# Optimization experiments

Measured on AMD Instinct MI355X. Metric: run time of the kernel, lower is better.

Reference implementation:

```python
import jax, jax.numpy as jnp
import numpy as np

# Dims (match init_kwargs)
T, C, RF, L = 32, 1, 64, 4096   # timesteps, inchannels, rf_size, length
K2 = 512                        # out_channels of self.ec
KWTA = 8
THRESH2 = 0.2                   # thresholds[1]
# inhibition_radius = 0 -> only per-feature inhibition in the winner loop


def setup_inputs() -> dict:
    key = jax.random.key(0)
    k1, k2 = jax.random.split(key)
    # spike-wave style input in [0,1)
    rec_field = jax.random.uniform(k1, (T, C, RF, L), dtype=jnp.float32)
    fan_in = C * RF * L
    weight = jax.random.normal(k2, (K2, C, RF, L), dtype=jnp.float32) / np.float32(np.sqrt(fan_in))
    return {"rec_field": rec_field, "weight": weight}


def reference(rec_field, weight):
    # LocalConvolution with kernel == full input -> single output location:
    # out[t, o, 0, 0] = sum_{c,h,w} rec_field[t,c,h,w] * weight[o,c,h,w]
    out = jnp.einsum('tchw,ochw->to', rec_field, weight)[:, :, None, None]  # (T, K2, 1, 1)

    # sf.fire(out, thresh2, True): zero potentials strictly below threshold
    pot = jnp.where(out < THRESH2, jnp.zeros_like(out), out)
    spikes = jnp.sign(pot)  # pot >= 0 after thresholding -> spikes in {0,1}

    # sf.get_k_winners(pot, kwta, inhibition_radius): spikes = pot.sign()
    n_t = spikes.shape[0]
    # index of earliest spike time (SpykeTorch cumulative-spike convention)
    first = jnp.clip((n_t - spikes.sum(axis=0, keepdims=True)).astype(jnp.int32), 0, n_t - 1)
    values = jnp.take_along_axis(pot, first, axis=0)          # (1, K2, 1, 1)
    trunc = spikes * values                                   # propagate earliest potential
    v = trunc.max() * n_t                                     # large offset so spiking neurons dominate
    trunc = trunc + spikes * v
    total = trunc.sum(axis=0)[:, 0, 0]                        # (K2,) -- spatial dims are 1x1

    # iterative k-WTA with per-feature inhibition (inhibition_radius=0; spatial is 1x1)
    sel = jnp.zeros((K2,), dtype=bool)
    t = total
    for _ in range(KWTA):  # small static loop
        idx = jnp.argmax(t)
        valid = t[idx] != 0          # original breaks when max == 0; totals are >= 0
        sel = sel.at[idx].set(sel[idx] | valid)
        t = t.at[idx].set(0.0)       # inhibit winning feature

    coef = sel.astype(pot.dtype)[None, :, None, None]
    return jnp.sign(pot * coef)  # (T, K2, 1, 1)
```

## Files before the change

### kernel.cpp

```cpp
#include <hip/hip_runtime.h>

#define TT    32
#define KDIM  262144
#define NFEAT 512
#define NFB   16
#define FPT   8
#define TPT   8
#define BK    256

__device__ __forceinline__ void async_ld16(const float* g, float* lds_row) {
    __builtin_amdgcn_global_load_lds(
        (const __attribute__((address_space(1))) unsigned int*)g,
        (__attribute__((address_space(3))) unsigned int*)lds_row, 16, 0, 0);
}

__global__ __launch_bounds__(512, 2)
void gemm_partial(const float* __restrict__ x, const float* __restrict__ w,
                  float* __restrict__ partial, int KC) {
    __shared__ float xs[2][TT][BK];

    const int tid  = threadIdx.x;
    const int lane = tid & 63;
    const int wave = tid >> 6;
    const int fgrp = wave & 1;
    const int tgrp = wave >> 1;
    const int ftile  = blockIdx.x;
    const int kchunk = blockIdx.y;
    const int f0 = ftile * NFB + fgrp * FPT;
    const int t0 = tgrp * TPT;
    const size_t kbase = (size_t)kchunk * (size_t)KC;

    float acc[FPT][TPT];
#pragma unroll
    for (int j = 0; j < FPT; ++j)
#pragma unroll
        for (int t = 0; t < TPT; ++t) acc[j][t] = 0.f;

    const float* wbase = w + (size_t)f0 * KDIM + kbase + (lane << 2);
    const float* xbase = x + kbase + (lane << 2);

#pragma unroll
    for (int r = 0; r < 4; ++r) {
        const int t = wave * 4 + r;
        async_ld16(xbase + (size_t)t * KDIM, &xs[0][t][0]);
    }

    int cur = 0;
    for (int ks = 0; ks < KC; ks += BK) {
        __syncthreads();

        if (ks + BK < KC) {
#pragma unroll
            for (int r = 0; r < 4; ++r) {
                const int t = wave * 4 + r;
                async_ld16(xbase + (size_t)t * KDIM + (ks + BK), &xs[cur ^ 1][t][0]);
            }
        }

        float4 wv[FPT];
#pragma unroll
        for (int j = 0; j < FPT; ++j)
            wv[j] = *(const float4*)(wbase + (size_t)j * KDIM + ks);

#pragma unroll
        for (int t = 0; t < TPT; ++t) {
            const float4 xv = *(const float4*)(&xs[cur][t0 + t][lane << 2]);
#pragma unroll
            for (int j = 0; j < FPT; ++j) {
                acc[j][t] = fmaf(wv[j].x, xv.x, acc[j][t]);
                acc[j][t] = fmaf(wv[j].y, xv.y, acc[j][t]);
                acc[j][t] = fmaf(wv[j].z, xv.z, acc[j][t]);
                acc[j][t] = fmaf(wv[j].w, xv.w, acc[j][t]);
            }
        }
        cur ^= 1;
    }

#pragma unroll
    for (int j = 0; j < FPT; ++j) {
#pragma unroll
        for (int t = 0; t < TPT; ++t) {
            float v = acc[j][t];
            v += __shfl_xor(v, 32, 64);
            v += __shfl_xor(v, 16, 64);
            v += __shfl_xor(v,  8, 64);
            v += __shfl_xor(v,  4, 64);
            v += __shfl_xor(v,  2, 64);
            v += __shfl_xor(v,  1, 64);
            acc[j][t] = v;
        }
    }

    if (lane == 0) {
#pragma unroll
        for (int j = 0; j < FPT; ++j) {
            float* p = partial + ((size_t)kchunk * NFEAT + (f0 + j)) * TT + t0;
            *(float4*)(p)     = make_float4(acc[j][0], acc[j][1], acc[j][2], acc[j][3]);
            *(float4*)(p + 4) = make_float4(acc[j][4], acc[j][5], acc[j][6], acc[j][7]);
        }
    }
}

__global__ __launch_bounds__(256)
void reduce_chunks(const float* __restrict__ partial, int nkc,
                   float* __restrict__ potraw) {
    const int id = blockIdx.x * 256 + threadIdx.x;
    float s = 0.f;
    for (int c = 0; c < nkc; ++c)
        s += partial[(size_t)c * (NFEAT * TT) + id];
    potraw[id] = s;
}

__global__ __launch_bounds__(512)
void finalize(const float* __restrict__ potraw, float* __restrict__ out) {
    const int o = threadIdx.x;

    float pot[TT];
#pragma unroll
    for (int t = 0; t < TT; ++t) {
        const float s = potraw[o * TT + t];
        pot[t] = (s < 0.2f) ? 0.f : s;
    }

    int cnt = 0;
#pragma unroll
    for (int t = 0; t < TT; ++t) cnt += (pot[t] > 0.f) ? 1 : 0;

    int first = TT - cnt;
    if (first > TT - 1) first = TT - 1;
    float value = 0.f;
#pragma unroll
    for (int t = 0; t < TT; ++t)
        if (t == first) value = pot[t];

    __shared__ float rv[NFEAT];
    __shared__ int   ri[NFEAT];
    __shared__ float tot[NFEAT];
    __shared__ int   sel[NFEAT];

    rv[o] = (cnt > 0) ? value : 0.f;
    __syncthreads();
    for (int s = 256; s > 0; s >>= 1) {
        if (o < s) rv[o] = fmaxf(rv[o], rv[o + s]);
        __syncthreads();
    }
    const float v = rv[0] * (float)TT;
    __syncthreads();

    tot[o] = (float)cnt * (value + v);
    sel[o] = 0;
    __syncthreads();

    for (int it = 0; it < 8; ++it) {
        rv[o] = tot[o]; ri[o] = o;
        __syncthreads();
        for (int s = 256; s > 0; s >>= 1) {
            if (o < s) {
                const float v2 = rv[o + s];
                const int   i2 = ri[o + s];
                if (v2 > rv[o] || (v2 == rv[o] && i2 < ri[o])) {
                    rv[o] = v2; ri[o] = i2;
                }
            }
            __syncthreads();
        }
        if (o == 0) {
            if (rv[0] != 0.f) sel[ri[0]] = 1;
            tot[ri[0]] = 0.f;
        }
        __syncthreads();
    }

#pragma unroll
    for (int t = 0; t < TT; ++t)
        out[t * NFEAT + o] = (sel[o] && pot[t] > 0.f) ? 1.f : 0.f;
}

extern "C" void kernel_launch(void* const* d_in, const int* in_sizes, int n_in,
                              void* d_out, int out_size, void* d_ws, size_t ws_size,
                              hipStream_t stream) {
    const float* x = (const float*)d_in[0];
    const float* w = (const float*)d_in[1];
    float* out = (float*)d_out;

    int nkc = 32;
    while (nkc > 1 &&
           ((size_t)(nkc + 1) * NFEAT * TT * sizeof(float)) > ws_size)
        nkc >>= 1;
    const int KC = KDIM / nkc;

    float* partial = (float*)d_ws;
    float* potraw  = partial + (size_t)nkc * NFEAT * TT;

    gemm_partial<<<dim3(32, nkc), 512, 0, stream>>>(x, w, partial, KC);
    reduce_chunks<<<(NFEAT * TT) / 256, 256, 0, stream>>>(partial, nkc, potraw);
    finalize<<<1, NFEAT, 0, stream>>>(potraw, out);
}
```

Baseline: 895.9 us.

## Stage weights through LDS with async loads and halve feature tile per block

```diff
diff --git a/kernel.cpp b/kernel.cpp
--- a/kernel.cpp
+++ b/kernel.cpp
@@ -3,8 +3,8 @@
 #define TT    32
 #define KDIM  262144
 #define NFEAT 512
-#define NFB   16
-#define FPT   8
+#define NFB   8
+#define FPT   4
 #define TPT   8
 #define BK    256
 
@@ -14,10 +14,11 @@
         (__attribute__((address_space(3))) unsigned int*)lds_row, 16, 0, 0);
 }
 
-__global__ __launch_bounds__(512, 2)
+__global__ __launch_bounds__(512, 4)
 void gemm_partial(const float* __restrict__ x, const float* __restrict__ w,
                   float* __restrict__ partial, int KC) {
     __shared__ float xs[2][TT][BK];
+    __shared__ float ws[2][NFB][BK];
 
     const int tid  = threadIdx.x;
     const int lane = tid & 63;
@@ -26,8 +27,10 @@
     const int tgrp = wave >> 1;
     const int ftile  = blockIdx.x;
     const int kchunk = blockIdx.y;
-    const int f0 = ftile * NFB + fgrp * FPT;
+    const int fbase = ftile * NFB;
+    const int f0 = fbase + fgrp * FPT;
     const int t0 = tgrp * TPT;
+    const int xrow = wave * 4;
     const size_t kbase = (size_t)kchunk * (size_t)KC;
 
     float acc[FPT][TPT];
@@ -36,45 +39,53 @@
 #pragma unroll
         for (int t = 0; t < TPT; ++t) acc[j][t] = 0.f;
 
-    const float* wbase = w + (size_t)f0 * KDIM + kbase + (lane << 2);
-    const float* xbase = x + kbase + (lane << 2);
-
-#pragma unroll
-    for (int r = 0; r < 4; ++r) {
-        const int t = wave * 4 + r;
-        async_ld16(xbase + (size_t)t * KDIM, &xs[0][t][0]);
-    }
-
-    int cur = 0;
-    for (int ks = 0; ks < KC; ks += BK) {
-        __syncthreads();
-
-        if (ks + BK < KC) {
-#pragma unroll
-            for (int r = 0; r < 4; ++r) {
-                const int t = wave * 4 + r;
-                async_ld16(xbase + (size_t)t * KDIM + (ks + BK), &xs[cur ^ 1][t][0]);
-            }
-        }
-
-        float4 wv[FPT];
-#pragma unroll
-        for (int j = 0; j < FPT; ++j)
-            wv[j] = *(const float4*)(wbase + (size_t)j * KDIM + ks);
-
-#pragma unroll
-        for (int t = 0; t < TPT; ++t) {
-            const float4 xv = *(const float4*)(&xs[cur][t0 + t][lane << 2]);
-#pragma unroll
-            for (int j = 0; j < FPT; ++j) {
-                acc[j][t] = fmaf(wv[j].x, xv.x, acc[j][t]);
-                acc[j][t] = fmaf(wv[j].y, xv.y, acc[j][t]);
-                acc[j][t] = fmaf(wv[j].z, xv.z, acc[j][t]);
-                acc[j][t] = fmaf(wv[j].w, xv.w, acc[j][t]);
-            }
-        }
-        cur ^= 1;
-    }
+    const float* xsrc = x + kbase + (lane << 2);
+    const float* wsrc = w + (size_t)(fbase + wave) * KDIM + kbase + (lane << 2);
+
+#pragma unroll
+    for (int r = 0; r < 4; ++r)
+        async_ld16(xsrc + (size_t)(xrow + r) * KDIM, &xs[0][xrow + r][0]);
+    async_ld16(wsrc, &ws[0][wave][0]);
+
+#define COMPUTE_STEP(buf)                                                     \
+    {                                                                         \
+        float4 wv[FPT];                                                       \
+        _Pragma("unroll")                                                     \
+        for (int j = 0; j < FPT; ++j)                                         \
+            wv[j] = *(const float4*)(&ws[buf][fgrp * FPT + j][lane << 2]);    \
+        _Pragma("unroll")                                                     \
+        for (int t = 0; t < TPT; ++t) {                                       \
+            const float4 xv = *(const float4*)(&xs[buf][t0 + t][lane << 2]);  \
+            _Pragma("unroll")                                                 \
+            for (int j = 0; j < FPT; ++j) {                                   \
+                acc[j][t] = fmaf(wv[j].x, xv.x, acc[j][t]);                   \
+                acc[j][t] = fmaf(wv[j].y, xv.y, acc[j][t]);                   \
+                acc[j][t] = fmaf(wv[j].z, xv.z, acc[j][t]);                   \
+                acc[j][t] = fmaf(wv[j].w, xv.w, acc[j][t]);                   \
+            }                                                                 \
+        }                                                                     \
+    }
+
+    for (int ks = 0; ks < KC; ks += 2 * BK) {
+        __syncthreads();
+#pragma unroll
+        for (int r = 0; r < 4; ++r)
+            async_ld16(xsrc + (size_t)(xrow + r) * KDIM + (ks + BK),
+                       &xs[1][xrow + r][0]);
+        async_ld16(wsrc + (ks + BK), &ws[1][wave][0]);
+        COMPUTE_STEP(0)
+
+        __syncthreads();
+        if (ks + 2 * BK < KC) {
+#pragma unroll
+            for (int r = 0; r < 4; ++r)
+                async_ld16(xsrc + (size_t)(xrow + r) * KDIM + (ks + 2 * BK),
+                           &xs[0][xrow + r][0]);
+            async_ld16(wsrc + (ks + 2 * BK), &ws[0][wave][0]);
+        }
+        COMPUTE_STEP(1)
+    }
+#undef COMPUTE_STEP
 
 #pragma unroll
     for (int j = 0; j < FPT; ++j) {
@@ -192,7 +203,7 @@
     float* partial = (float*)d_ws;
     float* potraw  = partial + (size_t)nkc * NFEAT * TT;
 
-    gemm_partial<<<dim3(32, nkc), 512, 0, stream>>>(x, w, partial, KC);
+    gemm_partial<<<dim3(NFEAT / NFB, nkc), 512, 0, stream>>>(x, w, partial, KC);
     reduce_chunks<<<(NFEAT * TT) / 256, 256, 0, stream>>>(partial, nkc, potraw);
     finalize<<<1, NFEAT, 0, stream>>>(potraw, out);
 }
```

Result: faster. 818.6 us (-8.6%).

## Triple-buffer weight and input tiles in LDS via async loads; wave-level k-WTA

Applied to the files above, without the earlier changes.

```diff
diff --git a/kernel.cpp b/kernel.cpp
--- a/kernel.cpp
+++ b/kernel.cpp
@@ -7,6 +7,7 @@
 #define FPT   8
 #define TPT   8
 #define BK    256
+#define NBUF  3
 
 __device__ __forceinline__ void async_ld16(const float* g, float* lds_row) {
     __builtin_amdgcn_global_load_lds(
@@ -17,7 +18,8 @@
 __global__ __launch_bounds__(512, 2)
 void gemm_partial(const float* __restrict__ x, const float* __restrict__ w,
                   float* __restrict__ partial, int KC) {
-    __shared__ float xs[2][TT][BK];
+    __shared__ float xs[NBUF][TT][BK];
+    __shared__ float ws[NBUF][NFB][BK];
 
     const int tid  = threadIdx.x;
     const int lane = tid & 63;
@@ -26,8 +28,11 @@
     const int tgrp = wave >> 1;
     const int ftile  = blockIdx.x;
     const int kchunk = blockIdx.y;
-    const int f0 = ftile * NFB + fgrp * FPT;
+    const int fbase = ftile * NFB;
+    const int f0 = fbase + fgrp * FPT;
     const int t0 = tgrp * TPT;
+    const int xrow = wave * 4;
+    const int wrow = wave * 2;
     const size_t kbase = (size_t)kchunk * (size_t)KC;
 
     float acc[FPT][TPT];
@@ -36,35 +41,29 @@
 #pragma unroll
         for (int t = 0; t < TPT; ++t) acc[j][t] = 0.f;
 
-    const float* wbase = w + (size_t)f0 * KDIM + kbase + (lane << 2);
-    const float* xbase = x + kbase + (lane << 2);
-
-#pragma unroll
-    for (int r = 0; r < 4; ++r) {
-        const int t = wave * 4 + r;
-        async_ld16(xbase + (size_t)t * KDIM, &xs[0][t][0]);
-    }
-
-    int cur = 0;
-    for (int ks = 0; ks < KC; ks += BK) {
-        __syncthreads();
-
-        if (ks + BK < KC) {
-#pragma unroll
-            for (int r = 0; r < 4; ++r) {
-                const int t = wave * 4 + r;
-                async_ld16(xbase + (size_t)t * KDIM + (ks + BK), &xs[cur ^ 1][t][0]);
-            }
-        }
-
+    const float* xsrc = x + kbase + (lane << 2);
+    const float* wsrc = w + kbase + (lane << 2);
+
+    auto stage = [&](int b, int step) {
+        const size_t ko = (size_t)step * BK;
+#pragma unroll
+        for (int r = 0; r < 4; ++r)
+            async_ld16(xsrc + (size_t)(xrow + r) * KDIM + ko, &xs[b][xrow + r][0]);
+#pragma unroll
+        for (int r = 0; r < 2; ++r)
+            async_ld16(wsrc + (size_t)(fbase + wrow + r) * KDIM + ko, &ws[b][wrow + r][0]);
+    };
+
+    auto compute = [&](int b) {
+        const float* xb = &xs[b][0][0];
+        const float* wb = &ws[b][0][0];
         float4 wv[FPT];
 #pragma unroll
         for (int j = 0; j < FPT; ++j)
-            wv[j] = *(const float4*)(wbase + (size_t)j * KDIM + ks);
-
+            wv[j] = *(const float4*)(wb + (fgrp * FPT + j) * BK + (lane << 2));
 #pragma unroll
         for (int t = 0; t < TPT; ++t) {
-            const float4 xv = *(const float4*)(&xs[cur][t0 + t][lane << 2]);
+            const float4 xv = *(const float4*)(xb + (t0 + t) * BK + (lane << 2));
 #pragma unroll
             for (int j = 0; j < FPT; ++j) {
                 acc[j][t] = fmaf(wv[j].x, xv.x, acc[j][t]);
@@ -73,8 +72,27 @@
                 acc[j][t] = fmaf(wv[j].w, xv.w, acc[j][t]);
             }
         }
-        cur ^= 1;
-    }
+    };
+
+    const int nsteps = KC / BK;
+
+    stage(0, 0);
+    stage(1, 1);
+
+    int buf = 0;
+    for (int i = 0; i < nsteps - 1; ++i) {
+        asm volatile("s_waitcnt vmcnt(6)" ::: "memory");
+        __builtin_amdgcn_s_barrier();
+        if (i + 2 < nsteps) {
+            int b2 = buf + 2; if (b2 >= NBUF) b2 -= NBUF;
+            stage(b2, i + 2);
+        }
+        compute(buf);
+        if (++buf == NBUF) buf = 0;
+    }
+    asm volatile("s_waitcnt vmcnt(0)" ::: "memory");
+    __builtin_amdgcn_s_barrier();
+    compute(buf);
 
 #pragma unroll
     for (int j = 0; j < FPT; ++j) {
@@ -134,42 +152,52 @@
         if (t == first) value = pot[t];
 
     __shared__ float rv[NFEAT];
-    __shared__ int   ri[NFEAT];
     __shared__ float tot[NFEAT];
     __shared__ int   sel[NFEAT];
-
-    rv[o] = (cnt > 0) ? value : 0.f;
-    __syncthreads();
-    for (int s = 256; s > 0; s >>= 1) {
-        if (o < s) rv[o] = fmaxf(rv[o], rv[o + s]);
-        __syncthreads();
-    }
-    const float v = rv[0] * (float)TT;
-    __syncthreads();
+    __shared__ float vbc;
+
+    rv[o]  = (cnt > 0) ? value : 0.f;
+    sel[o] = 0;
+    __syncthreads();
+
+    if (o < 64) {
+        float m = rv[o];
+#pragma unroll
+        for (int j = 1; j < 8; ++j) m = fmaxf(m, rv[o + 64 * j]);
+#pragma unroll
+        for (int s = 32; s; s >>= 1) m = fmaxf(m, __shfl_xor(m, s, 64));
+        if (o == 0) vbc = m * (float)TT;
+    }
+    __syncthreads();
+    const float v = vbc;
 
     tot[o] = (float)cnt * (value + v);
-    sel[o] = 0;
-    __syncthreads();
-
-    for (int it = 0; it < 8; ++it) {
-        rv[o] = tot[o]; ri[o] = o;
-        __syncthreads();
-        for (int s = 256; s > 0; s >>= 1) {
-            if (o < s) {
-                const float v2 = rv[o + s];
-                const int   i2 = ri[o + s];
-                if (v2 > rv[o] || (v2 == rv[o] && i2 < ri[o])) {
-                    rv[o] = v2; ri[o] = i2;
-                }
+    __syncthreads();
+
+    if (o < 64) {
+        float tv[8];
+#pragma unroll
+        for (int j = 0; j < 8; ++j) tv[j] = tot[o + 64 * j];
+        for (int it = 0; it < 8; ++it) {
+            float bv = tv[0]; int bi = o;
+#pragma unroll
+            for (int j = 1; j < 8; ++j) {
+                const int idx = o + 64 * j;
+                if (tv[j] > bv || (tv[j] == bv && idx < bi)) { bv = tv[j]; bi = idx; }
             }
-            __syncthreads();
-        }
-        if (o == 0) {
-            if (rv[0] != 0.f) sel[ri[0]] = 1;
-            tot[ri[0]] = 0.f;
-        }
-        __syncthreads();
-    }
+#pragma unroll
+            for (int s = 32; s; s >>= 1) {
+                const float ov = __shfl_xor(bv, s, 64);
+                const int   oi = __shfl_xor(bi, s, 64);
+                if (ov > bv || (ov == bv && oi < bi)) { bv = ov; bi = oi; }
+            }
+            if (bv != 0.f && o == (bi & 63)) sel[bi] = 1;
+#pragma unroll
+            for (int j = 0; j < 8; ++j)
+                if (o + 64 * j == bi) tv[j] = 0.f;
+        }
+    }
+    __syncthreads();
 
 #pragma unroll
     for (int t = 0; t < TT; ++t)
@@ -192,7 +220,7 @@
     float* partial = (float*)d_ws;
     float* potraw  = partial + (size_t)nkc * NFEAT * TT;
 
-    gemm_partial<<<dim3(32, nkc), 512, 0, stream>>>(x, w, partial, KC);
+    gemm_partial<<<dim3(NFEAT / NFB, nkc), 512, 0, stream>>>(x, w, partial, KC);
     reduce_chunks<<<(NFEAT * TT) / 256, 256, 0, stream>>>(partial, nkc, potraw);
     finalize<<<1, NFEAT, 0, stream>>>(potraw, out);
 }
```

After: 851.0 us. -5.0%, faster.
